# Kernel tuning notes

Measured on AMD Instinct MI355X. Metric: run time of the kernel, lower is better.

## Reference

```python
import jax, jax.numpy as jnp
import numpy as np

# ---- fixed architecture hyperparameters (match init_kwargs) ----
B, S = 4, 1024
L, H, DM, DF = 4, 8, 512, 2048
DH = DM // H          # 64 head dim (= 2*R after gated SPE filter)
NS = 5                # num_sines
R = 32                # num_realizations
M = 2 * DH            # favor_feature_dims = 128 (split as +/- of 64 projections)
LN_EPS = 1e-5
ATT_EPS = 1e-6


def layernorm(x, g, b):
    mu = x.mean(-1, keepdims=True)
    var = ((x - mu) ** 2).mean(-1, keepdims=True)
    return (x - mu) * jax.lax.rsqrt(var + LN_EPS) * g + b


def sine_spe(freqs, offsets, gains, noise, seq_len):
    """SineSPE positional code. freqs/offsets/gains: (H,DH,NS); noise: (H,DH,2NS,R).
    Returns qbar, kbar of shape (S,H,DH,R)."""
    pos = jnp.arange(seq_len, dtype=freqs.dtype)
    f = jax.nn.sigmoid(freqs)[:, :, None, :] / 2.0                       # (H,DH,1,NS)
    ph_q = 2.0 * jnp.pi * f * pos[None, None, :, None] + offsets[:, :, None, :]
    ph_k = 2.0 * jnp.pi * f * pos[None, None, :, None]
    om_q = jnp.stack([jnp.cos(ph_q), jnp.sin(ph_q)], -1).reshape(H, DH, seq_len, 2 * NS)
    om_k = jnp.stack([jnp.cos(ph_k), jnp.sin(ph_k)], -1).reshape(H, DH, seq_len, 2 * NS)
    g = jax.nn.softplus(gains)
    g = jnp.stack([g, g], -1).reshape(H, DH, 2 * NS)                      # upsample gains
    z = noise * g[..., None] / jnp.sqrt(jnp.asarray(2.0 * NS, freqs.dtype))
    qbar = jnp.einsum('hdsk,hdkr->shdr', om_q, z)
    kbar = jnp.einsum('hdsk,hdkr->shdr', om_k, z)
    scale = (R * DH) ** 0.25
    return qbar / scale, kbar / scale


def spe_filter(q, k, qbar, kbar, gate, gnoise):
    """Gated SPE filter. q,k: (B,S,H,DH); qbar/kbar: (S,H,DH,R); gate: (H,DH); gnoise: (H,DH,R).
    Returns qhat, khat of shape (B,S,H,2R)."""
    g = jax.nn.sigmoid(gate)[..., None]                                   # (H,DH,1)
    gn = gnoise / (DH * R) ** 0.25
    seq_len = qbar.shape[0]
    bias = jnp.broadcast_to(jnp.sqrt(g) * gn, (seq_len, H, DH, R))
    qb = jnp.concatenate([jnp.sqrt(1.0 - g) * qbar, bias], -1)            # (S,H,DH,2R)
    kb = jnp.concatenate([jnp.sqrt(1.0 - g) * kbar, bias], -1)
    qhat = jnp.einsum('bshd,shdr->bshr', q, qb)
    khat = jnp.einsum('bshd,shdr->bshr', k, kb)
    return qhat, khat


def favor(x, omega):
    """FAVOR+ softmax feature map. x: (B,S,H,DH); omega: (DH, M//2) -> (B,S,H,M)."""
    x = x * (DH ** -0.25)                                                 # sqrt(softmax_temp), temp=1/sqrt(DH)
    half_norm = 0.5 * jnp.sum(x * x, -1, keepdims=True)
    u = jnp.einsum('bshe,em->bshm', x, omega)
    phi = jnp.concatenate([jnp.exp(u - half_norm), jnp.exp(-u - half_norm)], -1)
    return phi / jnp.sqrt(jnp.asarray(M, x.dtype))


def causal_linear_attention(Q, K, V):
    """Causal linear (kernelized) attention via lax.scan. Q,K: (B,S,H,M); V: (B,S,H,DH)."""
    Bv = Q.shape[0]

    def step(carry, qkv):
        Skv, sk = carry
        q, k, v = qkv                                                     # (B,H,M),(B,H,M),(B,H,DH)
        Skv = Skv + jnp.einsum('bhm,bhd->bhmd', k, v)
        sk = sk + k
        num = jnp.einsum('bhm,bhmd->bhd', q, Skv)
        den = jnp.einsum('bhm,bhm->bh', q, sk) + ATT_EPS
        return (Skv, sk), num / den[..., None]

    init = (jnp.zeros((Bv, H, M, DH), Q.dtype), jnp.zeros((Bv, H, M), Q.dtype))
    xs = tuple(jnp.moveaxis(t, 1, 0) for t in (Q, K, V))
    _, out = jax.lax.scan(step, init, xs)
    return jnp.moveaxis(out, 0, 1)                                        # (B,S,H,DH)


def setup_inputs() -> dict:
    key = jax.random.key(0)
    ks = jax.random.split(key, 14)

    def rn(k, shape, scale=1.0):
        return jax.random.normal(k, shape, dtype=jnp.float32) * scale

    return {
        'x': rn(ks[0], (B, S, DM)),
        'Wq': rn(ks[1], (L, DM, DM), 0.02), 'bq': jnp.zeros((L, DM), jnp.float32),
        'Wk': rn(ks[2], (L, DM, DM), 0.02), 'bk': jnp.zeros((L, DM), jnp.float32),
        'Wv': rn(ks[3], (L, DM, DM), 0.02), 'bv': jnp.zeros((L, DM), jnp.float32),
        'Wo': rn(ks[4], (L, DM, DM), 0.02), 'bo': jnp.zeros((L, DM), jnp.float32),
        'W1': rn(ks[5], (L, DM, DF), 0.02), 'b1': jnp.zeros((L, DF), jnp.float32),
        'W2': rn(ks[6], (L, DF, DM), 0.02), 'b2': jnp.zeros((L, DM), jnp.float32),
        'ln1_g': jnp.ones((L, DM), jnp.float32), 'ln1_b': jnp.zeros((L, DM), jnp.float32),
        'ln2_g': jnp.ones((L, DM), jnp.float32), 'ln2_b': jnp.zeros((L, DM), jnp.float32),
        'spe_freqs': rn(ks[7], (L, H, DH, NS)),
        'spe_offsets': rn(ks[8], (L, H, DH, NS)),
        'spe_gains': rn(ks[9], (L, H, DH, NS)),
        'spe_noise': rn(ks[10], (L, H, DH, 2 * NS, R)),
        'gate': rn(ks[11], (L, H, DH)),
        'gate_noise': rn(ks[12], (L, H, DH, R)),
        'favor_omega': rn(ks[13], (L, DH, M // 2)),
    }


def reference(x, Wq, bq, Wk, bk, Wv, bv, Wo, bo, W1, b1, W2, b2,
              ln1_g, ln1_b, ln2_g, ln2_b,
              spe_freqs, spe_offsets, spe_gains, spe_noise, gate, gate_noise, favor_omega):
    Bv, Sv, _ = x.shape
    out = x
    for l in range(L):
        qbar, kbar = sine_spe(spe_freqs[l], spe_offsets[l], spe_gains[l], spe_noise[l], Sv)
        q = (out @ Wq[l] + bq[l]).reshape(Bv, Sv, H, DH)
        k = (out @ Wk[l] + bk[l]).reshape(Bv, Sv, H, DH)
        v = (out @ Wv[l] + bv[l]).reshape(Bv, Sv, H, DH)
        qh, kh = spe_filter(q, k, qbar, kbar, gate[l], gate_noise[l])
        Qf = favor(qh, favor_omega[l])
        Kf = favor(kh, favor_omega[l])
        att = causal_linear_attention(Qf, Kf, v).reshape(Bv, Sv, DM)
        att = att @ Wo[l] + bo[l]
        h = layernorm(out + att, ln1_g[l], ln1_b[l])
        y = jax.nn.relu(h @ W1[l] + b1[l]) @ W2[l] + b2[l]
        out = layernorm(h + y, ln2_g[l], ln2_b[l])
    return out
```

## Files before the change

### kernel.cpp

```cpp
#include <hip/hip_runtime.h>
#include <math.h>

#define BB 4
#define SS 1024
#define LL 4
#define HH 8
#define DM 512
#define DF 2048
#define DH 64
#define NS 5
#define RR 32
#define MM 128
#define NC 16
#define CHK 64
#define QKV_N 1536

#define INV_SQRT10   0.316227766016838f
#define INV_SCALE    0.148650889375340f
#define TEMP_SCALE   0.353553390593274f
#define INV_SQRT_M   0.088388347648318f
#define TWO_PI       6.283185307179586f

typedef __attribute__((ext_vector_type(8))) short bf16x8;
typedef __attribute__((ext_vector_type(4))) float f32x4;

__device__ __forceinline__ unsigned short f2bf(float f) {
  union { float f; unsigned int u; } v; v.f = f;
  unsigned int r = v.u + 0x7FFFu + ((v.u >> 16) & 1u);
  return (unsigned short)(r >> 16);
}

__device__ __forceinline__ float bf2f(unsigned short u) {
  union { unsigned int u; float f; } v; v.u = (unsigned int)u << 16;
  return v.f;
}

__device__ __forceinline__ void gld_lds16(const unsigned short* g, unsigned short* l) {
  __builtin_amdgcn_global_load_lds((const __attribute__((address_space(1))) void*)g,
                                   (__attribute__((address_space(3))) void*)l,
                                   16, 0, 0);
}

template<int RELU, int OUT_BF>
__global__ __launch_bounds__(256)
void gemm_mfma(const unsigned short* __restrict__ A, const unsigned short* __restrict__ Bt,
               const float* __restrict__ bias, float* __restrict__ Cf,
               unsigned short* __restrict__ Cbf, int M, int N, int K)
{
  __shared__ unsigned short As[128 * 32];
  __shared__ unsigned short Bs[128 * 32];
  const int tid  = threadIdx.x;
  const int w    = tid >> 6;
  const int lane = tid & 63;
  const int row0 = blockIdx.y * 128;
  const int col0 = blockIdx.x * 128;
  const int wr = (w >> 1) * 64;
  const int wc = (w & 1) * 64;
  const int c0 = w * 2, c1 = w * 2 + 1;
  const int m0 = c0 * 16 + (lane >> 2);
  const int m1 = c1 * 16 + (lane >> 2);
  const int kA = (lane & 3) * 8;

  f32x4 acc[4][4] = {};

  for (int k0 = 0; k0 < K; k0 += 32) {
    gld_lds16(&A [(size_t)(row0 + m0) * K + k0 + kA], &As[c0 * 512]);
    gld_lds16(&A [(size_t)(row0 + m1) * K + k0 + kA], &As[c1 * 512]);
    gld_lds16(&Bt[(size_t)(col0 + m0) * K + k0 + kA], &Bs[c0 * 512]);
    gld_lds16(&Bt[(size_t)(col0 + m1) * K + k0 + kA], &Bs[c1 * 512]);
    __syncthreads();
    const int rA = wr + (lane & 15);
    const int rB = wc + (lane & 15);
    const int kk = (lane >> 4) * 8;
    bf16x8 af[4], bfr[4];
#pragma unroll
    for (int i = 0; i < 4; ++i) {
      af[i]  = *reinterpret_cast<const bf16x8*>(&As[(rA + i * 16) * 32 + kk]);
      bfr[i] = *reinterpret_cast<const bf16x8*>(&Bs[(rB + i * 16) * 32 + kk]);
    }
#pragma unroll
    for (int mi = 0; mi < 4; ++mi)
#pragma unroll
      for (int ni = 0; ni < 4; ++ni)
        acc[mi][ni] = __builtin_amdgcn_mfma_f32_16x16x32_bf16(af[mi], bfr[ni], acc[mi][ni], 0, 0, 0);
    __syncthreads();
  }
  const int cr = (lane >> 4) * 4;
  const int cc = lane & 15;
#pragma unroll
  for (int mi = 0; mi < 4; ++mi) {
#pragma unroll
    for (int ni = 0; ni < 4; ++ni) {
      const int col = col0 + wc + ni * 16 + cc;
      const float bv = bias[col];
#pragma unroll
      for (int r = 0; r < 4; ++r) {
        const int row = row0 + wr + mi * 16 + cr + r;
        float v = acc[mi][ni][r] + bv;
        if (RELU) v = fmaxf(v, 0.f);
        if (OUT_BF) Cbf[(size_t)row * N + col] = f2bf(v);
        else        Cf [(size_t)row * N + col] = v;
      }
    }
  }
}

template<int RELU, int OUT_BF>
__global__ __launch_bounds__(256)
void gemm_mfma_n64(const unsigned short* __restrict__ A, const unsigned short* __restrict__ Bt,
                   const float* __restrict__ bias, float* __restrict__ Cf,
                   unsigned short* __restrict__ Cbf, int M, int N, int K)
{
  __shared__ unsigned short As[128 * 32];
  __shared__ unsigned short Bs[64 * 32];
  const int tid  = threadIdx.x;
  const int w    = tid >> 6;
  const int lane = tid & 63;
  const int row0 = blockIdx.y * 128;
  const int col0 = blockIdx.x * 64;
  const int wr = (w >> 1) * 64;
  const int wc = (w & 1) * 32;
  const int c0 = w * 2, c1 = w * 2 + 1;
  const int m0 = c0 * 16 + (lane >> 2);
  const int m1 = c1 * 16 + (lane >> 2);
  const int mb = w * 16 + (lane >> 2);
  const int kA = (lane & 3) * 8;

  f32x4 acc[4][2] = {};

  for (int k0 = 0; k0 < K; k0 += 32) {
    gld_lds16(&A [(size_t)(row0 + m0) * K + k0 + kA], &As[c0 * 512]);
    gld_lds16(&A [(size_t)(row0 + m1) * K + k0 + kA], &As[c1 * 512]);
    gld_lds16(&Bt[(size_t)(col0 + mb) * K + k0 + kA], &Bs[w * 512]);
    __syncthreads();
    const int rA = wr + (lane & 15);
    const int rB = wc + (lane & 15);
    const int kk = (lane >> 4) * 8;
    bf16x8 af[4], bfr[2];
#pragma unroll
    for (int i = 0; i < 4; ++i)
      af[i]  = *reinterpret_cast<const bf16x8*>(&As[(rA + i * 16) * 32 + kk]);
#pragma unroll
    for (int i = 0; i < 2; ++i)
      bfr[i] = *reinterpret_cast<const bf16x8*>(&Bs[(rB + i * 16) * 32 + kk]);
#pragma unroll
    for (int mi = 0; mi < 4; ++mi)
#pragma unroll
      for (int ni = 0; ni < 2; ++ni)
        acc[mi][ni] = __builtin_amdgcn_mfma_f32_16x16x32_bf16(af[mi], bfr[ni], acc[mi][ni], 0, 0, 0);
    __syncthreads();
  }
  const int cr = (lane >> 4) * 4;
  const int cc = lane & 15;
#pragma unroll
  for (int mi = 0; mi < 4; ++mi) {
#pragma unroll
    for (int ni = 0; ni < 2; ++ni) {
      const int col = col0 + wc + ni * 16 + cc;
      const float bv = bias[col];
#pragma unroll
      for (int r = 0; r < 4; ++r) {
        const int row = row0 + wr + mi * 16 + cr + r;
        float v = acc[mi][ni][r] + bv;
        if (RELU) v = fmaxf(v, 0.f);
        if (OUT_BF) Cbf[(size_t)row * N + col] = f2bf(v);
        else        Cf [(size_t)row * N + col] = v;
      }
    }
  }
}

__global__ __launch_bounds__(256)
void transpose_bf(const float* __restrict__ W, unsigned short* __restrict__ Wt, int K, int N,
                  size_t inStride, size_t outStride)
{
  const float* Wl = W + blockIdx.z * inStride;
  unsigned short* Wtl = Wt + blockIdx.z * outStride;
  __shared__ float tile[32][33];
  const int k0 = blockIdx.y * 32, n0 = blockIdx.x * 32;
  const int tx = threadIdx.x & 31, ty = threadIdx.x >> 5;
#pragma unroll
  for (int j = 0; j < 4; ++j)
    tile[ty + 8 * j][tx] = Wl[(size_t)(k0 + ty + 8 * j) * N + n0 + tx];
  __syncthreads();
#pragma unroll
  for (int j = 0; j < 4; ++j)
    Wtl[(size_t)(n0 + ty + 8 * j) * K + k0 + tx] = f2bf(tile[tx][ty + 8 * j]);
}

__global__ __launch_bounds__(256)
void pack_bias(const float* __restrict__ bq, const float* __restrict__ bk,
               const float* __restrict__ bv, float* __restrict__ out)
{
  const int l = blockIdx.y;
  const int i = blockIdx.x * 256 + threadIdx.x;
  if (i < QKV_N)
    out[l * QKV_N + i] = (i < 512) ? bq[l * DM + i] : (i < 1024) ? bk[l * DM + i - 512]
                                                                 : bv[l * DM + i - 1024];
}

__global__ __launch_bounds__(256)
void cvt_bf16(const float* __restrict__ in, unsigned short* __restrict__ out, int n4)
{
  const int i = blockIdx.x * 256 + threadIdx.x;
  if (i < n4) {
    const float4 v = reinterpret_cast<const float4*>(in)[i];
    ushort4 o;
    o.x = f2bf(v.x); o.y = f2bf(v.y); o.z = f2bf(v.z); o.w = f2bf(v.w);
    reinterpret_cast<ushort4*>(out)[i] = o;
  }
}

__global__ __launch_bounds__(256)
void spe_prep_all(const float* __restrict__ gains, const float* __restrict__ noise,
                  const float* __restrict__ gate, const float* __restrict__ gnoise,
                  const float* __restrict__ offsets,
                  float* __restrict__ zpf, unsigned short* __restrict__ wbb,
                  float2* __restrict__ offcs)
{
  const int i = blockIdx.x * 256 + threadIdx.x;
  const int NZ = LL * HH * RR * 10 * DH;
  const int NW = LL * HH * RR * DH;
  const int NO = LL * HH * DH * NS;
  if (i < NZ) {
    const int d = i & 63;
    int j = i >> 6;
    const int k = j % 10; j /= 10;
    const int r = j & 31; j >>= 5;
    const int h = j & 7;  const int l = j >> 3;
    const int lhd = (l * HH + h) * DH + d;
    const float ga = gains[lhd * NS + (k >> 1)];
    const float sp = (ga > 20.f) ? ga : log1pf(__expf(ga));
    const float gg = 1.f / (1.f + __expf(-gate[lhd]));
    const float c1 = sqrtf(fmaxf(1.f - gg, 0.f));
    const float nz = noise[((size_t)lhd * 10 + k) * 32 + r];
    zpf[i] = nz * sp * c1 * (INV_SQRT10 * INV_SCALE * TEMP_SCALE);
  } else if (i < NZ + NW) {
    int j = i - NZ;
    const int d = j & 63; j >>= 6;
    const int r = j & 31; j >>= 5;
    const int h = j & 7;  const int l = j >> 3;
    const int lhd = (l * HH + h) * DH + d;
    const float gg = 1.f / (1.f + __expf(-gate[lhd]));
    wbb[i - NZ] = f2bf(sqrtf(gg) * gnoise[(size_t)lhd * 32 + r] * (INV_SCALE * TEMP_SCALE));
  } else if (i < NZ + NW + NO) {
    const int j = i - NZ - NW;
    float sn, cn;
    __sincosf(offsets[j], &sn, &cn);
    offcs[j] = make_float2(cn, sn);
  }
}

__global__ __launch_bounds__(256)
void spe_xhat(const float* __restrict__ freqs, const float2* __restrict__ offcs,
              const float* __restrict__ zpf, const unsigned short* __restrict__ wbb,
              const unsigned short* __restrict__ qkvb,
              unsigned short* __restrict__ xhat, float* __restrict__ hn)
{
  const int s = blockIdx.x;
  const int h = blockIdx.y;
  const int t = threadIdx.x;
  const int w = t >> 6;
  const int lane = t & 63;
  __shared__ float omqT[10][64];
  __shared__ float omkT[10][64];
  __shared__ unsigned short qbT[64 * 64];
  __shared__ unsigned short kbT[64 * 64];
  __shared__ unsigned short rQ[16 * 64];
  __shared__ unsigned short rK[16 * 64];
  __shared__ float hqp[4][8];

  for (int e = t; e < DH * NS; e += 256) {
    const int d = e / NS, ns = e - d * NS;
    const float fr = 0.5f / (1.f + __expf(-freqs[(h * DH + d) * NS + ns]));
    float sn, cn;
    __sincosf(TWO_PI * fr * (float)s, &sn, &cn);
    const float2 oc = offcs[(h * DH + d) * NS + ns];
    omkT[2 * ns][d]     = cn;
    omkT[2 * ns + 1][d] = sn;
    omqT[2 * ns][d]     = cn * oc.x - sn * oc.y;
    omqT[2 * ns + 1][d] = sn * oc.x + cn * oc.y;
  }
  if (t < 64) {
    const int isK = t >> 5;
    const int b = (t >> 3) & 3;
    const int j = t & 7;
    const unsigned short* src = qkvb + ((size_t)b * SS + s) * QKV_N + isK * 512 + h * DH + j * 8;
    unsigned short* dst = (isK ? rK : rQ) + b * 64 + ((j ^ b) << 3);
    *reinterpret_cast<bf16x8*>(dst) = *reinterpret_cast<const bf16x8*>(src);
  } else if (t < 256) {
    const int i = t - 64;
    bf16x8 z = {};
    if (i < 96) *reinterpret_cast<bf16x8*>(&rQ[256 + i * 8]) = z;
    else        *reinterpret_cast<bf16x8*>(&rK[256 + (i - 96) * 8]) = z;
  }
  __syncthreads();
  {
    const int r = t >> 3, d0 = (t & 7) * 8;
    float accq[8] = {}, acck[8] = {};
    const float* zr = zpf + (size_t)(h * RR + r) * 640 + d0;
#pragma unroll
    for (int k = 0; k < 10; ++k) {
      const float4 z0 = *reinterpret_cast<const float4*>(zr + k * 64);
      const float4 z1 = *reinterpret_cast<const float4*>(zr + k * 64 + 4);
      const float4 oq0 = *reinterpret_cast<const float4*>(&omqT[k][d0]);
      const float4 oq1 = *reinterpret_cast<const float4*>(&omqT[k][d0 + 4]);
      const float4 ok0 = *reinterpret_cast<const float4*>(&omkT[k][d0]);
      const float4 ok1 = *reinterpret_cast<const float4*>(&omkT[k][d0 + 4]);
      accq[0] += z0.x * oq0.x; accq[1] += z0.y * oq0.y;
      accq[2] += z0.z * oq0.z; accq[3] += z0.w * oq0.w;
      accq[4] += z1.x * oq1.x; accq[5] += z1.y * oq1.y;
      accq[6] += z1.z * oq1.z; accq[7] += z1.w * oq1.w;
      acck[0] += z0.x * ok0.x; acck[1] += z0.y * ok0.y;
      acck[2] += z0.z * ok0.z; acck[3] += z0.w * ok0.w;
      acck[4] += z1.x * ok1.x; acck[5] += z1.y * ok1.y;
      acck[6] += z1.z * ok1.z; acck[7] += z1.w * ok1.w;
    }
    bf16x8 qv, kv;
#pragma unroll
    for (int j = 0; j < 8; ++j) {
      qv[j] = (short)f2bf(accq[j]);
      kv[j] = (short)f2bf(acck[j]);
    }
    const int sd0 = d0 ^ ((r & 7) << 3);
    *reinterpret_cast<bf16x8*>(&qbT[r * 64 + sd0]) = qv;
    *reinterpret_cast<bf16x8*>(&kbT[r * 64 + sd0]) = kv;
    const bf16x8 wv = *reinterpret_cast<const bf16x8*>(&wbb[(size_t)(h * RR + r) * 64 + d0]);
    *reinterpret_cast<bf16x8*>(&qbT[(32 + r) * 64 + sd0]) = wv;
    *reinterpret_cast<bf16x8*>(&kbT[(32 + r) * 64 + sd0]) = wv;
  }
  __syncthreads();
  f32x4 aq = {0.f, 0.f, 0.f, 0.f}, ak = {0.f, 0.f, 0.f, 0.f};
  const int arow = lane & 15;
  const int colr = w * 16 + (lane & 15);
#pragma unroll
  for (int kt = 0; kt < 2; ++kt) {
    const int g = kt * 4 + (lane >> 4);
    const bf16x8 fAq = *reinterpret_cast<const bf16x8*>(&rQ[arow * 64 + ((g ^ (arow & 7)) << 3)]);
    const bf16x8 fAk = *reinterpret_cast<const bf16x8*>(&rK[arow * 64 + ((g ^ (arow & 7)) << 3)]);
    const bf16x8 fBq = *reinterpret_cast<const bf16x8*>(&qbT[colr * 64 + ((g ^ (colr & 7)) << 3)]);
    const bf16x8 fBk = *reinterpret_cast<const bf16x8*>(&kbT[colr * 64 + ((g ^ (colr & 7)) << 3)]);
    aq = __builtin_amdgcn_mfma_f32_16x16x32_bf16(fAq, fBq, aq, 0, 0, 0);
    ak = __builtin_amdgcn_mfma_f32_16x16x32_bf16(fAk, fBk, ak, 0, 0, 0);
  }
  float rq[4], rk2[4];
#pragma unroll
  for (int r = 0; r < 4; ++r) { rq[r] = aq[r] * aq[r]; rk2[r] = ak[r] * ak[r]; }
#pragma unroll
  for (int off = 1; off < 16; off <<= 1) {
#pragma unroll
    for (int r = 0; r < 4; ++r) {
      rq[r]  += __shfl_xor(rq[r],  off, 64);
      rk2[r] += __shfl_xor(rk2[r], off, 64);
    }
  }
  if (lane == 0) {
#pragma unroll
    for (int r = 0; r < 4; ++r) { hqp[w][r] = rq[r]; hqp[w][4 + r] = rk2[r]; }
  }
  if (lane < 16) {
#pragma unroll
    for (int r = 0; r < 4; ++r) {
      const size_t rowq = ((size_t)r * SS + s) * HH + h;
      xhat[rowq * 64 + w * 16 + lane] = f2bf(aq[r]);
      xhat[(rowq + (size_t)BB * SS * HH) * 64 + w * 16 + lane] = f2bf(ak[r]);
    }
  }
  __syncthreads();
  if (t < 8) {
    const int b = t & 3;
    const int ko = (t >> 2) * 4;
    const float v = 0.5f * (hqp[0][ko + b] + hqp[1][ko + b] + hqp[2][ko + b] + hqp[3][ko + b]);
    const size_t row = ((size_t)b * SS + s) * HH + h + (size_t)(t >> 2) * BB * SS * HH;
    hn[row] = v;
  }
}

__global__ __launch_bounds__(256)
void favor_gemm(const unsigned short* __restrict__ xhat, const unsigned short* __restrict__ omgT,
                const float* __restrict__ hn, unsigned short* __restrict__ QfKfB)
{
  __shared__ unsigned short As[128 * 32];
  __shared__ unsigned short Bs[64 * 32];
  const int tid  = threadIdx.x;
  const int w    = tid >> 6;
  const int lane = tid & 63;
  const int row0 = blockIdx.x * 128;
  const int c0 = w * 2, c1 = w * 2 + 1;
  const int m0 = c0 * 16 + (lane >> 2);
  const int m1 = c1 * 16 + (lane >> 2);
  const int mb = w * 16 + (lane >> 2);
  const int kA = (lane & 3) * 8;

  f32x4 acc[2][4] = {};

  for (int k0 = 0; k0 < 64; k0 += 32) {
    gld_lds16(&xhat[(size_t)(row0 + m0) * 64 + k0 + kA], &As[c0 * 512]);
    gld_lds16(&xhat[(size_t)(row0 + m1) * 64 + k0 + kA], &As[c1 * 512]);
    gld_lds16(&omgT[(size_t)mb * 64 + k0 + kA], &Bs[w * 512]);
    __syncthreads();
    const int rA = w * 32 + (lane & 15);
    const int kk = (lane >> 4) * 8;
    bf16x8 af[2], bfr[4];
#pragma unroll
    for (int i = 0; i < 2; ++i)
      af[i]  = *reinterpret_cast<const bf16x8*>(&As[(rA + i * 16) * 32 + kk]);
#pragma unroll
    for (int i = 0; i < 4; ++i)
      bfr[i] = *reinterpret_cast<const bf16x8*>(&Bs[(i * 16 + (lane & 15)) * 32 + kk]);
#pragma unroll
    for (int mi = 0; mi < 2; ++mi)
#pragma unroll
      for (int ni = 0; ni < 4; ++ni)
        acc[mi][ni] = __builtin_amdgcn_mfma_f32_16x16x32_bf16(af[mi], bfr[ni], acc[mi][ni], 0, 0, 0);
    __syncthreads();
  }
  const int cr = (lane >> 4) * 4;
  const int cc = lane & 15;
#pragma unroll
  for (int mi = 0; mi < 2; ++mi) {
#pragma unroll
    for (int r = 0; r < 4; ++r) {
      const size_t row = row0 + w * 32 + mi * 16 + cr + r;
      const float hnv = hn[row];
#pragma unroll
      for (int ni = 0; ni < 4; ++ni) {
        const int m = ni * 16 + cc;
        const float u = acc[mi][ni][r];
        QfKfB[row * MM + m]      = f2bf(__expf( u - hnv) * INV_SQRT_M);
        QfKfB[row * MM + m + 64] = f2bf(__expf(-u - hnv) * INV_SQRT_M);
      }
    }
  }
}

__global__ __launch_bounds__(256)
void attn_chunk_sums(const unsigned short* __restrict__ KfB, const unsigned short* __restrict__ qkvb,
                     float* __restrict__ Sch, float* __restrict__ kch)
{
  const int c = blockIdx.x, h = blockIdx.y, b = blockIdx.z;
  const int tid = threadIdx.x;
  const int w = tid >> 6, lane = tid & 63;
  __shared__ unsigned short KcT[128 * 64];
  __shared__ unsigned short VT[64 * 64];
  const size_t srow0 = (size_t)b * SS + c * CHK;

  for (int i = tid; i < 1024; i += 256) {
    const int m = i & 127, oct = i >> 7;
    const unsigned short* src = KfB + ((srow0 + oct * 8) * HH + h) * MM + m;
    bf16x8 v;
#pragma unroll
    for (int j = 0; j < 8; ++j) v[j] = (short)src[(size_t)j * (HH * MM)];
    *reinterpret_cast<bf16x8*>(&KcT[m * 64 + ((oct << 3) ^ ((m & 7) << 3))]) = v;
  }
  for (int i = tid; i < 512; i += 256) {
    const int d = i & 63, oct = i >> 6;
    const unsigned short* src = qkvb + (srow0 + oct * 8) * QKV_N + 1024 + h * DH + d;
    bf16x8 v;
#pragma unroll
    for (int j = 0; j < 8; ++j) v[j] = (short)src[(size_t)j * QKV_N];
    *reinterpret_cast<bf16x8*>(&VT[d * 64 + ((oct << 3) ^ ((d & 7) << 3))]) = v;
  }
  __syncthreads();

  const int kk = (lane >> 4) * 8;
  f32x4 acc[4][2] = {};
#pragma unroll
  for (int kc = 0; kc < 2; ++kc) {
    const int k = kc * 32 + kk;
#pragma unroll
    for (int di = 0; di < 4; ++di) {
      const int dA = di * 16 + (lane & 15);
      const bf16x8 a = *reinterpret_cast<const bf16x8*>(&VT[dA * 64 + (k ^ ((dA & 7) << 3))]);
#pragma unroll
      for (int mi = 0; mi < 2; ++mi) {
        const int mB = w * 32 + mi * 16 + (lane & 15);
        const bf16x8 bb = *reinterpret_cast<const bf16x8*>(&KcT[mB * 64 + (k ^ ((mB & 7) << 3))]);
        acc[di][mi] = __builtin_amdgcn_mfma_f32_16x16x32_bf16(a, bb, acc[di][mi], 0, 0, 0);
      }
    }
  }
  const size_t base = (((size_t)b * HH + h) * NC + c);
  float* So = Sch + base * (MM * DH);
  const int cr = (lane >> 4) * 4, cc = lane & 15;
#pragma unroll
  for (int di = 0; di < 4; ++di)
#pragma unroll
    for (int mi = 0; mi < 2; ++mi)
#pragma unroll
      for (int r = 0; r < 4; ++r)
        So[(size_t)(di * 16 + cr + r) * MM + (w * 32 + mi * 16 + cc)] = acc[di][mi][r];
  {
    const int m = tid >> 1, half = tid & 1;
    float ks = 0.f;
#pragma unroll
    for (int j = 0; j < 32; ++j) {
      const int t2 = half * 32 + j;
      ks += bf2f(KcT[m * 64 + (t2 ^ ((m & 7) << 3))]);
    }
    ks += __shfl_xor(ks, 1, 64);
    if (half == 0) kch[base * MM + m] = ks;
  }
}

__global__ __launch_bounds__(256)
void attn_scan(float* __restrict__ Sch, float* __restrict__ kch)
{
  const int bh = blockIdx.x, part = blockIdx.y;
  const int t = threadIdx.x;
  float* base = Sch + (size_t)bh * NC * (MM * DH);
  for (int e = part * 1024 + t; e < (part + 1) * 1024; e += 256) {
    float run = 0.f;
#pragma unroll
    for (int c = 0; c < NC; ++c) {
      const float v = base[(size_t)c * (MM * DH) + e];
      base[(size_t)c * (MM * DH) + e] = run;
      run += v;
    }
  }
  if (part == 0 && t < MM) {
    float* kb2 = kch + (size_t)bh * NC * MM;
    float run = 0.f;
#pragma unroll
    for (int c = 0; c < NC; ++c) {
      const float v = kb2[c * MM + t];
      kb2[c * MM + t] = run;
      run += v;
    }
  }
}

__global__ __launch_bounds__(256)
void attn_out(const unsigned short* __restrict__ QfKfB, const unsigned short* __restrict__ qkvb,
              const float* __restrict__ Sch, const float* __restrict__ kch,
              unsigned short* __restrict__ att)
{
  const int c = blockIdx.x, h = blockIdx.y, b = blockIdx.z;
  const int tid = threadIdx.x;
  const int w = tid >> 6;
  const int lane = tid & 63;
  __shared__ unsigned short Qc[64 * 128];
  __shared__ unsigned short Sb[64 * 64];
  __shared__ unsigned short KVU[12288];
  __shared__ float skp[MM];
  __shared__ float denl[64];

  unsigned short* Kc   = KVU;
  unsigned short* SpxT = KVU;
  unsigned short* VT   = KVU + 8192;

  const size_t srow0 = (size_t)b * SS + c * CHK;
  const unsigned short* Qg = QfKfB + (srow0 * HH + h) * MM;
  const unsigned short* Kg = Qg + (size_t)BB * SS * HH * MM;

  if (tid < MM) skp[tid] = kch[(((size_t)b * HH + h) * NC + c) * MM + tid];

  for (int i = tid; i < 1024; i += 256) {
    const int s2 = i >> 4, m8 = (i & 15) * 8;
    const int sw = m8 ^ ((s2 & 15) << 3);
    *reinterpret_cast<bf16x8*>(&Qc[s2 * 128 + sw]) =
        *reinterpret_cast<const bf16x8*>(&Qg[(size_t)s2 * (HH * MM) + m8]);
    *reinterpret_cast<bf16x8*>(&Kc[s2 * 128 + sw]) =
        *reinterpret_cast<const bf16x8*>(&Kg[(size_t)s2 * (HH * MM) + m8]);
  }
  for (int i = tid; i < 512; i += 256) {
    const int d = i & 63, oct = i >> 6;
    const unsigned short* src = qkvb + (srow0 + oct * 8) * QKV_N + 1024 + h * DH + d;
    bf16x8 v;
#pragma unroll
    for (int j = 0; j < 8; ++j) v[j] = (short)src[(size_t)j * QKV_N];
    *reinterpret_cast<bf16x8*>(&VT[d * 64 + ((oct << 3) ^ ((d & 7) << 3))]) = v;
  }
  __syncthreads();

  const int sA = w * 16 + (lane & 15);
  const int kk = (lane >> 4) * 8;
  f32x4 acc_s[4] = {};
#pragma unroll
  for (int kc = 0; kc < 4; ++kc) {
    const int k = kc * 32 + kk;
    const bf16x8 aq = *reinterpret_cast<const bf16x8*>(&Qc[sA * 128 + (k ^ ((sA & 15) << 3))]);
#pragma unroll
    for (int n = 0; n < 4; ++n) {
      const int tB = n * 16 + (lane & 15);
      const bf16x8 bq = *reinterpret_cast<const bf16x8*>(&Kc[tB * 128 + (k ^ ((tB & 15) << 3))]);
      acc_s[n] = __builtin_amdgcn_mfma_f32_16x16x32_bf16(aq, bq, acc_s[n], 0, 0, 0);
    }
  }
  __syncthreads();

  {
    const int g = lane >> 4;
    const int tcol = lane & 15;
    float dintra[4] = {0.f, 0.f, 0.f, 0.f};
#pragma unroll
    for (int r = 0; r < 4; ++r) {
      const int s = w * 16 + g * 4 + r;
#pragma unroll
      for (int n = 0; n < 4; ++n) {
        const int t2 = n * 16 + tcol;
        const float v = (t2 <= s) ? acc_s[n][r] : 0.f;
        dintra[r] += v;
        Sb[s * 64 + (t2 ^ ((s & 7) << 3))] = f2bf(v);
      }
    }
#pragma unroll
    for (int off = 1; off < 16; off <<= 1)
#pragma unroll
      for (int r = 0; r < 4; ++r) dintra[r] += __shfl_xor(dintra[r], off, 64);
    if (tcol == 0) {
#pragma unroll
      for (int r = 0; r < 4; ++r) denl[w * 16 + g * 4 + r] = dintra[r];
    }
  }
  {
    const float* Sp = Sch + (((size_t)b * HH + h) * NC + c) * (MM * DH);
    for (int i = tid; i < 1024; i += 256) {
      const int d = i >> 4, mo = (i & 15) * 8;
      const float4 a0 = *reinterpret_cast<const float4*>(Sp + (size_t)d * MM + mo);
      const float4 a1 = *reinterpret_cast<const float4*>(Sp + (size_t)d * MM + mo + 4);
      bf16x8 v;
      v[0] = (short)f2bf(a0.x); v[1] = (short)f2bf(a0.y);
      v[2] = (short)f2bf(a0.z); v[3] = (short)f2bf(a0.w);
      v[4] = (short)f2bf(a1.x); v[5] = (short)f2bf(a1.y);
      v[6] = (short)f2bf(a1.z); v[7] = (short)f2bf(a1.w);
      *reinterpret_cast<bf16x8*>(&SpxT[d * 128 + (mo ^ ((d & 15) << 3))]) = v;
    }
  }
  __syncthreads();

  f32x4 acc_o[4] = {};
#pragma unroll
  for (int kc = 0; kc < 2; ++kc) {
    const int k = kc * 32 + kk;
    const bf16x8 as = *reinterpret_cast<const bf16x8*>(&Sb[sA * 64 + (k ^ ((sA & 7) << 3))]);
#pragma unroll
    for (int n = 0; n < 4; ++n) {
      const int dB = n * 16 + (lane & 15);
      const bf16x8 bv = *reinterpret_cast<const bf16x8*>(&VT[dB * 64 + (k ^ ((dB & 7) << 3))]);
      acc_o[n] = __builtin_amdgcn_mfma_f32_16x16x32_bf16(as, bv, acc_o[n], 0, 0, 0);
    }
  }
#pragma unroll
  for (int kc = 0; kc < 4; ++kc) {
    const int k = kc * 32 + kk;
    const bf16x8 aq = *reinterpret_cast<const bf16x8*>(&Qc[sA * 128 + (k ^ ((sA & 15) << 3))]);
#pragma unroll
    for (int n = 0; n < 4; ++n) {
      const int dB = n * 16 + (lane & 15);
      const bf16x8 bs = *reinterpret_cast<const bf16x8*>(&SpxT[dB * 128 + (k ^ ((dB & 15) << 3))]);
      acc_o[n] = __builtin_amdgcn_mfma_f32_16x16x32_bf16(aq, bs, acc_o[n], 0, 0, 0);
    }
  }
  {
    const int s2 = tid >> 2, part = tid & 3;
    float p = 0.f;
#pragma unroll
    for (int j = 0; j < 32; ++j) {
      const int m = part * 32 + j;
      p += bf2f(Qc[s2 * 128 + (m ^ ((s2 & 15) << 3))]) * skp[m];
    }
    p += __shfl_xor(p, 1, 64);
    p += __shfl_xor(p, 2, 64);
    if (part == 0) denl[s2] += p + 1e-6f;
  }
  __syncthreads();

  {
    const int g = lane >> 4;
    const int dcol = lane & 15;
#pragma unroll
    for (int r = 0; r < 4; ++r) {
      const int s = w * 16 + g * 4 + r;
      const float dinv = 1.f / denl[s];
#pragma unroll
      for (int n = 0; n < 4; ++n)
        att[(srow0 + s) * DM + h * DH + n * 16 + dcol] = f2bf(acc_o[n][r] * dinv);
    }
  }
}

template<int WBF>
__global__ __launch_bounds__(256)
void add_ln(const float* __restrict__ a, const float* __restrict__ bres,
            const float* __restrict__ g, const float* __restrict__ be,
            float* __restrict__ out, unsigned short* __restrict__ outbf)
{
  const int row = blockIdx.x;
  const int t = threadIdx.x;
  const size_t base = (size_t)row * DM;
  const float x0 = a[base + t] + bres[base + t];
  const float x1 = a[base + t + 256] + bres[base + t + 256];
  __shared__ float red[8];
  float ssum = x0 + x1;
#pragma unroll
  for (int off = 32; off > 0; off >>= 1) ssum += __shfl_xor(ssum, off, 64);
  const int wid = t >> 6, lid = t & 63;
  if (lid == 0) red[wid] = ssum;
  __syncthreads();
  const float mu = (red[0] + red[1] + red[2] + red[3]) * (1.f / DM);
  const float d0 = x0 - mu, d1 = x1 - mu;
  float sv = d0 * d0 + d1 * d1;
#pragma unroll
  for (int off = 32; off > 0; off >>= 1) sv += __shfl_xor(sv, off, 64);
  if (lid == 0) red[4 + wid] = sv;
  __syncthreads();
  const float var = (red[4] + red[5] + red[6] + red[7]) * (1.f / DM);
  const float rs = rsqrtf(var + 1e-5f);
  const float o0 = d0 * rs * g[t]       + be[t];
  const float o1 = d1 * rs * g[t + 256] + be[t + 256];
  out[base + t]       = o0;
  out[base + t + 256] = o1;
  if (WBF) {
    outbf[base + t]       = f2bf(o0);
    outbf[base + t + 256] = f2bf(o1);
  }
}

extern "C" void kernel_launch(void* const* d_in, const int* in_sizes, int n_in,
                              void* d_out, int out_size, void* d_ws, size_t ws_size,
                              hipStream_t stream)
{
  const float* x      = (const float*)d_in[0];
  const float* Wq     = (const float*)d_in[1];
  const float* bq     = (const float*)d_in[2];
  const float* Wk     = (const float*)d_in[3];
  const float* bk     = (const float*)d_in[4];
  const float* Wv     = (const float*)d_in[5];
  const float* bv     = (const float*)d_in[6];
  const float* Wo     = (const float*)d_in[7];
  const float* bo     = (const float*)d_in[8];
  const float* W1     = (const float*)d_in[9];
  const float* b1     = (const float*)d_in[10];
  const float* W2     = (const float*)d_in[11];
  const float* b2     = (const float*)d_in[12];
  const float* ln1g   = (const float*)d_in[13];
  const float* ln1b   = (const float*)d_in[14];
  const float* ln2g   = (const float*)d_in[15];
  const float* ln2b   = (const float*)d_in[16];
  const float* freqs  = (const float*)d_in[17];
  const float* offs   = (const float*)d_in[18];
  const float* gains  = (const float*)d_in[19];
  const float* noise  = (const float*)d_in[20];
  const float* gate   = (const float*)d_in[21];
  const float* gnoise = (const float*)d_in[22];
  const float* omega  = (const float*)d_in[23];

  float* ws = (float*)d_ws;
  size_t o = 0;
  float* curf = ws + o; o += (size_t)BB * SS * DM;
  unsigned short* qkvb = (unsigned short*)(ws + o); o += (size_t)BB * SS * QKV_N / 2;
  float* Sch  = ws + o; o += (size_t)BB * HH * NC * MM * DH;
  float* kch  = ws + o; o += (size_t)BB * HH * NC * MM;
  float* hn   = ws + o; o += (size_t)2 * BB * SS * HH;
  float* bqkv = ws + o; o += (size_t)LL * QKV_N;
  float2* offcs = (float2*)(ws + o); o += (size_t)LL * HH * DH * NS * 2;
  float* zpf  = ws + o; o += (size_t)LL * HH * RR * 10 * DH;
  unsigned short* QfKfB = (unsigned short*)(ws + o); o += (size_t)2 * BB * SS * HH * MM / 2;
  unsigned short* xhat  = (unsigned short*)(ws + o); o += (size_t)2 * BB * SS * HH * DH / 2;
  unsigned short* attb  = (unsigned short*)(ws + o); o += (size_t)BB * SS * DM / 2;
  unsigned short* h_bf  = (unsigned short*)(ws + o); o += (size_t)BB * SS * DM / 2;
  unsigned short* curbf = (unsigned short*)(ws + o); o += (size_t)BB * SS * DM / 2;
  unsigned short* Wqkvt = (unsigned short*)(ws + o); o += (size_t)LL * QKV_N * DM / 2;
  unsigned short* Wot   = (unsigned short*)(ws + o); o += (size_t)LL * DM * DM / 2;
  unsigned short* W1t   = (unsigned short*)(ws + o); o += (size_t)DF * DM / 2;
  unsigned short* W2t   = (unsigned short*)(ws + o); o += (size_t)DM * DF / 2;
  unsigned short* omgT  = (unsigned short*)(ws + o); o += (size_t)LL * 4096 / 2;
  unsigned short* wbb   = (unsigned short*)(ws + o); o += (size_t)LL * HH * RR * DH / 2;

  float* attp = (float*)qkvb;
  float* hbuf = Sch;
  float* ybuf = Sch + (size_t)2 * 1024 * 1024;
  unsigned short* midbf = QfKfB;
  unsigned short* KfB   = QfKfB + (size_t)BB * SS * HH * MM;

  const int MROWS = BB * SS;

  cvt_bf16<<<(BB * SS * DM / 4 + 255) / 256, 256, 0, stream>>>(x, curbf, BB * SS * DM / 4);
  spe_prep_all<<<2856, 256, 0, stream>>>(gains, noise, gate, gnoise, offs, zpf, wbb, offcs);
  transpose_bf<<<dim3(16, 16, 4), 256, 0, stream>>>(Wq, Wqkvt,                     DM, DM, (size_t)DM * DM, (size_t)QKV_N * DM);
  transpose_bf<<<dim3(16, 16, 4), 256, 0, stream>>>(Wk, Wqkvt + (size_t)512 * DM,  DM, DM, (size_t)DM * DM, (size_t)QKV_N * DM);
  transpose_bf<<<dim3(16, 16, 4), 256, 0, stream>>>(Wv, Wqkvt + (size_t)1024 * DM, DM, DM, (size_t)DM * DM, (size_t)QKV_N * DM);
  transpose_bf<<<dim3(16, 16, 4), 256, 0, stream>>>(Wo, Wot, DM, DM, (size_t)DM * DM, (size_t)DM * DM);
  transpose_bf<<<dim3(2, 2, 4),   256, 0, stream>>>(omega, omgT, DH, MM / 2, (size_t)DH * (MM / 2), 4096);
  pack_bias<<<dim3(6, 4), 256, 0, stream>>>(bq, bk, bv, bqkv);

  for (int l = 0; l < LL; ++l) {
    const float* in = (l == 0) ? x : curf;

    gemm_mfma_n64<0, 1><<<dim3(QKV_N / 64, MROWS / 128), 256, 0, stream>>>(
        curbf, Wqkvt + (size_t)l * QKV_N * DM, bqkv + (size_t)l * QKV_N,
        (float*)nullptr, qkvb, MROWS, QKV_N, DM);

    spe_xhat<<<dim3(SS, HH), 256, 0, stream>>>(
        freqs + (size_t)l * HH * DH * NS, offcs + (size_t)l * HH * DH * NS,
        zpf + (size_t)l * HH * RR * 10 * DH, wbb + (size_t)l * HH * RR * DH,
        qkvb, xhat, hn);
    favor_gemm<<<dim3(2 * BB * SS * HH / 128), 256, 0, stream>>>(
        xhat, omgT + (size_t)l * 4096, hn, QfKfB);

    attn_chunk_sums<<<dim3(NC, HH, BB), 256, 0, stream>>>(KfB, qkvb, Sch, kch);
    attn_scan<<<dim3(BB * HH, 8), 256, 0, stream>>>(Sch, kch);
    attn_out<<<dim3(NC, HH, BB), 256, 0, stream>>>(QfKfB, qkvb, Sch, kch, attb);

    gemm_mfma_n64<0, 0><<<dim3(DM / 64, MROWS / 128), 256, 0, stream>>>(
        attb, Wot + (size_t)l * DM * DM, bo + (size_t)l * DM,
        attp, (unsigned short*)nullptr, MROWS, DM, DM);

    add_ln<1><<<MROWS, 256, 0, stream>>>(in, attp, ln1g + (size_t)l * DM, ln1b + (size_t)l * DM, hbuf, h_bf);

    transpose_bf<<<dim3(64, 16, 1), 256, 0, stream>>>(W1 + (size_t)l * DM * DF, W1t, DM, DF, 0, 0);
    gemm_mfma<1, 1><<<dim3(DF / 128, MROWS / 128), 256, 0, stream>>>(
        h_bf, W1t, b1 + (size_t)l * DF, (float*)nullptr, midbf, MROWS, DF, DM);
    transpose_bf<<<dim3(16, 64, 1), 256, 0, stream>>>(W2 + (size_t)l * DF * DM, W2t, DF, DM, 0, 0);
    gemm_mfma_n64<0, 0><<<dim3(DM / 64, MROWS / 128), 256, 0, stream>>>(
        midbf, W2t, b2 + (size_t)l * DM, ybuf, (unsigned short*)nullptr, MROWS, DM, DF);

    if (l == LL - 1) {
      add_ln<0><<<MROWS, 256, 0, stream>>>(hbuf, ybuf, ln2g + (size_t)l * DM, ln2b + (size_t)l * DM,
                                           (float*)d_out, (unsigned short*)nullptr);
    } else {
      add_ln<1><<<MROWS, 256, 0, stream>>>(hbuf, ybuf, ln2g + (size_t)l * DM, ln2b + (size_t)l * DM,
                                           curf, curbf);
    }
  }
}
```

Before: 747.9 us.

## Process eight positions per spe_xhat block with LDS-staged bf16 SPE noise

Each spe_xhat block now handles SG=8 consecutive sequence positions instead of one. The per-head z-matrix is stored pre-swizzled in bf16 and loaded once into LDS via gld_lds16, then reused across the eight positions. The sine/cosine terms are advanced with an angle-addition recurrence instead of a fresh sincos per position. This cuts repeated global z loads, the fp32 z traffic and transcendental work, but leaves only 1024 blocks, adds about 40KB of LDS per block (lowering occupancy), serialises positions with barriers, and adds bf16 rounding to z plus recurrence drift.

```diff
diff --git a/kernel.cpp b/kernel.cpp
--- a/kernel.cpp
+++ b/kernel.cpp
@@ -14,6 +14,7 @@
 #define NC 16
 #define CHK 64
 #define QKV_N 1536
+#define SG 8
 
 #define INV_SQRT10   0.316227766016838f
 #define INV_SCALE    0.148650889375340f
@@ -215,7 +216,7 @@
 void spe_prep_all(const float* __restrict__ gains, const float* __restrict__ noise,
                   const float* __restrict__ gate, const float* __restrict__ gnoise,
                   const float* __restrict__ offsets,
-                  float* __restrict__ zpf, unsigned short* __restrict__ wbb,
+                  unsigned short* __restrict__ zpb, unsigned short* __restrict__ wbb,
                   float2* __restrict__ offcs)
 {
   const int i = blockIdx.x * 256 + threadIdx.x;
@@ -234,7 +235,8 @@
     const float gg = 1.f / (1.f + __expf(-gate[lhd]));
     const float c1 = sqrtf(fmaxf(1.f - gg, 0.f));
     const float nz = noise[((size_t)lhd * 10 + k) * 32 + r];
-    zpf[i] = nz * sp * c1 * (INV_SQRT10 * INV_SCALE * TEMP_SCALE);
+    const int dsw = d ^ ((r & 7) << 3);
+    zpb[(i & ~63) | dsw] = f2bf(nz * sp * c1 * (INV_SQRT10 * INV_SCALE * TEMP_SCALE));
   } else if (i < NZ + NW) {
     int j = i - NZ;
     const int d = j & 63; j >>= 6;
@@ -253,125 +255,162 @@
 
 __global__ __launch_bounds__(256)
 void spe_xhat(const float* __restrict__ freqs, const float2* __restrict__ offcs,
-              const float* __restrict__ zpf, const unsigned short* __restrict__ wbb,
+              const unsigned short* __restrict__ zpb, const unsigned short* __restrict__ wbb,
               const unsigned short* __restrict__ qkvb,
               unsigned short* __restrict__ xhat, float* __restrict__ hn)
 {
-  const int s = blockIdx.x;
-  const int h = blockIdx.y;
-  const int t = threadIdx.x;
-  const int w = t >> 6;
+  const int s0 = blockIdx.x * SG;
+  const int h  = blockIdx.y;
+  const int t  = threadIdx.x;
+  const int w  = t >> 6;
   const int lane = t & 63;
+
+  __shared__ unsigned short zbS[RR * 10 * DH];
   __shared__ float omqT[10][64];
   __shared__ float omkT[10][64];
   __shared__ unsigned short qbT[64 * 64];
   __shared__ unsigned short kbT[64 * 64];
-  __shared__ unsigned short rQ[16 * 64];
-  __shared__ unsigned short rK[16 * 64];
-  __shared__ float hqp[4][8];
-
-  for (int e = t; e < DH * NS; e += 256) {
-    const int d = e / NS, ns = e - d * NS;
-    const float fr = 0.5f / (1.f + __expf(-freqs[(h * DH + d) * NS + ns]));
-    float sn, cn;
-    __sincosf(TWO_PI * fr * (float)s, &sn, &cn);
-    const float2 oc = offcs[(h * DH + d) * NS + ns];
-    omkT[2 * ns][d]     = cn;
-    omkT[2 * ns + 1][d] = sn;
-    omqT[2 * ns][d]     = cn * oc.x - sn * oc.y;
-    omqT[2 * ns + 1][d] = sn * oc.x + cn * oc.y;
-  }
+  __shared__ unsigned short rQall[SG][4][64];
+  __shared__ unsigned short rKall[SG][4][64];
+  __shared__ float hqp[SG][4][8];
+
+  {
+    const unsigned short* zsrc = zpb + (size_t)h * (RR * 10 * DH);
+#pragma unroll
+    for (int i = 0; i < 10; ++i)
+      gld_lds16(&zsrc[(size_t)(i * 256 + t) * 8], &zbS[(i * 256 + w * 64) * 8]);
+  }
+  for (int i = t; i < SG * 4 * 2 * 8; i += 256) {
+    const int oct = i & 7, qk = (i >> 3) & 1, b = (i >> 4) & 3, s = i >> 6;
+    const unsigned short* src = qkvb + ((size_t)b * SS + s0 + s) * QKV_N + qk * 512 + h * DH + oct * 8;
+    unsigned short* dst = (qk ? &rKall[s][b][0] : &rQall[s][b][0]) + ((oct ^ b) << 3);
+    *reinterpret_cast<bf16x8*>(dst) = *reinterpret_cast<const bf16x8*>(src);
+  }
+  {
+    const int r = t >> 3, oct = t & 7;
+    const bf16x8 wv = *reinterpret_cast<const bf16x8*>(&wbb[((size_t)h * RR + r) * 64 + oct * 8]);
+    const int sd = (oct ^ (r & 7)) << 3;
+    *reinterpret_cast<bf16x8*>(&qbT[(32 + r) * 64 + sd]) = wv;
+    *reinterpret_cast<bf16x8*>(&kbT[(32 + r) * 64 + sd]) = wv;
+  }
+  float ck[NS], sk[NS], cw[NS], sw[NS], ocx[NS], ocy[NS];
   if (t < 64) {
-    const int isK = t >> 5;
-    const int b = (t >> 3) & 3;
-    const int j = t & 7;
-    const unsigned short* src = qkvb + ((size_t)b * SS + s) * QKV_N + isK * 512 + h * DH + j * 8;
-    unsigned short* dst = (isK ? rK : rQ) + b * 64 + ((j ^ b) << 3);
-    *reinterpret_cast<bf16x8*>(dst) = *reinterpret_cast<const bf16x8*>(src);
-  } else if (t < 256) {
-    const int i = t - 64;
-    bf16x8 z = {};
-    if (i < 96) *reinterpret_cast<bf16x8*>(&rQ[256 + i * 8]) = z;
-    else        *reinterpret_cast<bf16x8*>(&rK[256 + (i - 96) * 8]) = z;
+    const int d = t;
+#pragma unroll
+    for (int ns = 0; ns < NS; ++ns) {
+      const float fr = 0.5f / (1.f + __expf(-freqs[(h * DH + d) * NS + ns]));
+      const float om = TWO_PI * fr;
+      __sincosf(om * (float)s0, &sk[ns], &ck[ns]);
+      __sincosf(om, &sw[ns], &cw[ns]);
+      const float2 oc = offcs[(h * DH + d) * NS + ns];
+      ocx[ns] = oc.x; ocy[ns] = oc.y;
+      omkT[2 * ns][d]     = ck[ns];
+      omkT[2 * ns + 1][d] = sk[ns];
+      omqT[2 * ns][d]     = ck[ns] * oc.x - sk[ns] * oc.y;
+      omqT[2 * ns + 1][d] = sk[ns] * oc.x + ck[ns] * oc.y;
+    }
   }
   __syncthreads();
-  {
-    const int r = t >> 3, d0 = (t & 7) * 8;
-    float accq[8] = {}, acck[8] = {};
-    const float* zr = zpf + (size_t)(h * RR + r) * 640 + d0;
-#pragma unroll
-    for (int k = 0; k < 10; ++k) {
-      const float4 z0 = *reinterpret_cast<const float4*>(zr + k * 64);
-      const float4 z1 = *reinterpret_cast<const float4*>(zr + k * 64 + 4);
-      const float4 oq0 = *reinterpret_cast<const float4*>(&omqT[k][d0]);
-      const float4 oq1 = *reinterpret_cast<const float4*>(&omqT[k][d0 + 4]);
-      const float4 ok0 = *reinterpret_cast<const float4*>(&omkT[k][d0]);
-      const float4 ok1 = *reinterpret_cast<const float4*>(&omkT[k][d0 + 4]);
-      accq[0] += z0.x * oq0.x; accq[1] += z0.y * oq0.y;
-      accq[2] += z0.z * oq0.z; accq[3] += z0.w * oq0.w;
-      accq[4] += z1.x * oq1.x; accq[5] += z1.y * oq1.y;
-      accq[6] += z1.z * oq1.z; accq[7] += z1.w * oq1.w;
-      acck[0] += z0.x * ok0.x; acck[1] += z0.y * ok0.y;
-      acck[2] += z0.z * ok0.z; acck[3] += z0.w * ok0.w;
-      acck[4] += z1.x * ok1.x; acck[5] += z1.y * ok1.y;
-      acck[6] += z1.z * ok1.z; acck[7] += z1.w * ok1.w;
-    }
-    bf16x8 qv, kv;
-#pragma unroll
-    for (int j = 0; j < 8; ++j) {
-      qv[j] = (short)f2bf(accq[j]);
-      kv[j] = (short)f2bf(acck[j]);
-    }
-    const int sd0 = d0 ^ ((r & 7) << 3);
-    *reinterpret_cast<bf16x8*>(&qbT[r * 64 + sd0]) = qv;
-    *reinterpret_cast<bf16x8*>(&kbT[r * 64 + sd0]) = kv;
-    const bf16x8 wv = *reinterpret_cast<const bf16x8*>(&wbb[(size_t)(h * RR + r) * 64 + d0]);
-    *reinterpret_cast<bf16x8*>(&qbT[(32 + r) * 64 + sd0]) = wv;
-    *reinterpret_cast<bf16x8*>(&kbT[(32 + r) * 64 + sd0]) = wv;
-  }
-  __syncthreads();
-  f32x4 aq = {0.f, 0.f, 0.f, 0.f}, ak = {0.f, 0.f, 0.f, 0.f};
+
   const int arow = lane & 15;
+  const int brow = arow & 3;
   const int colr = w * 16 + (lane & 15);
-#pragma unroll
-  for (int kt = 0; kt < 2; ++kt) {
-    const int g = kt * 4 + (lane >> 4);
-    const bf16x8 fAq = *reinterpret_cast<const bf16x8*>(&rQ[arow * 64 + ((g ^ (arow & 7)) << 3)]);
-    const bf16x8 fAk = *reinterpret_cast<const bf16x8*>(&rK[arow * 64 + ((g ^ (arow & 7)) << 3)]);
-    const bf16x8 fBq = *reinterpret_cast<const bf16x8*>(&qbT[colr * 64 + ((g ^ (colr & 7)) << 3)]);
-    const bf16x8 fBk = *reinterpret_cast<const bf16x8*>(&kbT[colr * 64 + ((g ^ (colr & 7)) << 3)]);
-    aq = __builtin_amdgcn_mfma_f32_16x16x32_bf16(fAq, fBq, aq, 0, 0, 0);
-    ak = __builtin_amdgcn_mfma_f32_16x16x32_bf16(fAk, fBk, ak, 0, 0, 0);
-  }
-  float rq[4], rk2[4];
-#pragma unroll
-  for (int r = 0; r < 4; ++r) { rq[r] = aq[r] * aq[r]; rk2[r] = ak[r] * ak[r]; }
-#pragma unroll
-  for (int off = 1; off < 16; off <<= 1) {
-#pragma unroll
-    for (int r = 0; r < 4; ++r) {
-      rq[r]  += __shfl_xor(rq[r],  off, 64);
-      rk2[r] += __shfl_xor(rk2[r], off, 64);
-    }
-  }
-  if (lane == 0) {
-#pragma unroll
-    for (int r = 0; r < 4; ++r) { hqp[w][r] = rq[r]; hqp[w][4 + r] = rk2[r]; }
-  }
-  if (lane < 16) {
-#pragma unroll
-    for (int r = 0; r < 4; ++r) {
-      const size_t rowq = ((size_t)r * SS + s) * HH + h;
-      xhat[rowq * 64 + w * 16 + lane] = f2bf(aq[r]);
-      xhat[(rowq + (size_t)BB * SS * HH) * 64 + w * 16 + lane] = f2bf(ak[r]);
-    }
-  }
-  __syncthreads();
-  if (t < 8) {
-    const int b = t & 3;
-    const int ko = (t >> 2) * 4;
-    const float v = 0.5f * (hqp[0][ko + b] + hqp[1][ko + b] + hqp[2][ko + b] + hqp[3][ko + b]);
-    const size_t row = ((size_t)b * SS + s) * HH + h + (size_t)(t >> 2) * BB * SS * HH;
+
+  for (int si = 0; si < SG; ++si) {
+    {
+      const int r = t >> 3, oct = t & 7, d0 = oct * 8;
+      float accq[8] = {}, acck[8] = {};
+      const unsigned short* zr = &zbS[r * 640 + ((oct ^ (r & 7)) << 3)];
+#pragma unroll
+      for (int k = 0; k < 10; ++k) {
+        const bf16x8 zv = *reinterpret_cast<const bf16x8*>(&zr[k * 64]);
+        float zf[8];
+#pragma unroll
+        for (int j = 0; j < 8; ++j) zf[j] = bf2f((unsigned short)zv[j]);
+        const float4 oq0 = *reinterpret_cast<const float4*>(&omqT[k][d0]);
+        const float4 oq1 = *reinterpret_cast<const float4*>(&omqT[k][d0 + 4]);
+        const float4 ok0 = *reinterpret_cast<const float4*>(&omkT[k][d0]);
+        const float4 ok1 = *reinterpret_cast<const float4*>(&omkT[k][d0 + 4]);
+        accq[0] += zf[0] * oq0.x; accq[1] += zf[1] * oq0.y;
+        accq[2] += zf[2] * oq0.z; accq[3] += zf[3] * oq0.w;
+        accq[4] += zf[4] * oq1.x; accq[5] += zf[5] * oq1.y;
+        accq[6] += zf[6] * oq1.z; accq[7] += zf[7] * oq1.w;
+        acck[0] += zf[0] * ok0.x; acck[1] += zf[1] * ok0.y;
+        acck[2] += zf[2] * ok0.z; acck[3] += zf[3] * ok0.w;
+        acck[4] += zf[4] * ok1.x; acck[5] += zf[5] * ok1.y;
+        acck[6] += zf[6] * ok1.z; acck[7] += zf[7] * ok1.w;
+      }
+      bf16x8 qv, kv;
+#pragma unroll
+      for (int j = 0; j < 8; ++j) {
+        qv[j] = (short)f2bf(accq[j]);
+        kv[j] = (short)f2bf(acck[j]);
+      }
+      const int sd0 = d0 ^ ((r & 7) << 3);
+      *reinterpret_cast<bf16x8*>(&qbT[r * 64 + sd0]) = qv;
+      *reinterpret_cast<bf16x8*>(&kbT[r * 64 + sd0]) = kv;
+    }
+    __syncthreads();
+
+    f32x4 aq = {0.f, 0.f, 0.f, 0.f}, ak = {0.f, 0.f, 0.f, 0.f};
+    const bf16x8 zerov = {};
+#pragma unroll
+    for (int kt = 0; kt < 2; ++kt) {
+      const int g = kt * 4 + (lane >> 4);
+      const bf16x8 rq = *reinterpret_cast<const bf16x8*>(&rQall[si][brow][(g ^ brow) << 3]);
+      const bf16x8 rk = *reinterpret_cast<const bf16x8*>(&rKall[si][brow][(g ^ brow) << 3]);
+      const bf16x8 fAq = (arow < 4) ? rq : zerov;
+      const bf16x8 fAk = (arow < 4) ? rk : zerov;
+      const bf16x8 fBq = *reinterpret_cast<const bf16x8*>(&qbT[colr * 64 + ((g ^ (colr & 7)) << 3)]);
+      const bf16x8 fBk = *reinterpret_cast<const bf16x8*>(&kbT[colr * 64 + ((g ^ (colr & 7)) << 3)]);
+      aq = __builtin_amdgcn_mfma_f32_16x16x32_bf16(fAq, fBq, aq, 0, 0, 0);
+      ak = __builtin_amdgcn_mfma_f32_16x16x32_bf16(fAk, fBk, ak, 0, 0, 0);
+    }
+    {
+      float rq2[4], rk2[4];
+#pragma unroll
+      for (int r = 0; r < 4; ++r) { rq2[r] = aq[r] * aq[r]; rk2[r] = ak[r] * ak[r]; }
+#pragma unroll
+      for (int off = 1; off < 16; off <<= 1) {
+#pragma unroll
+        for (int r = 0; r < 4; ++r) {
+          rq2[r] += __shfl_xor(rq2[r], off, 64);
+          rk2[r] += __shfl_xor(rk2[r], off, 64);
+        }
+      }
+      if (lane == 0) {
+#pragma unroll
+        for (int r = 0; r < 4; ++r) { hqp[si][w][r] = rq2[r]; hqp[si][w][4 + r] = rk2[r]; }
+      }
+    }
+    if (lane < 16) {
+#pragma unroll
+      for (int r = 0; r < 4; ++r) {
+        const size_t rowq = ((size_t)r * SS + s0 + si) * HH + h;
+        xhat[rowq * 64 + w * 16 + lane] = f2bf(aq[r]);
+        xhat[(rowq + (size_t)BB * SS * HH) * 64 + w * 16 + lane] = f2bf(ak[r]);
+      }
+    }
+    if (si < SG - 1 && t < 64) {
+      const int d = t;
+#pragma unroll
+      for (int ns = 0; ns < NS; ++ns) {
+        const float c2 = ck[ns] * cw[ns] - sk[ns] * sw[ns];
+        const float s2 = sk[ns] * cw[ns] + ck[ns] * sw[ns];
+        ck[ns] = c2; sk[ns] = s2;
+        omkT[2 * ns][d]     = c2;
+        omkT[2 * ns + 1][d] = s2;
+        omqT[2 * ns][d]     = c2 * ocx[ns] - s2 * ocy[ns];
+        omqT[2 * ns + 1][d] = s2 * ocx[ns] + c2 * ocy[ns];
+      }
+    }
+    __syncthreads();
+  }
+
+  if (t < 64) {
+    const int si = t >> 3, j = t & 7, qk = j >> 2, b = j & 3;
+    const float v = 0.5f * (hqp[si][0][j] + hqp[si][1][j] + hqp[si][2][j] + hqp[si][3][j]);
+    const size_t row = ((size_t)b * SS + s0 + si) * HH + h + (size_t)qk * (BB * SS * HH);
     hn[row] = v;
   }
 }
@@ -755,7 +794,7 @@
   float* hn   = ws + o; o += (size_t)2 * BB * SS * HH;
   float* bqkv = ws + o; o += (size_t)LL * QKV_N;
   float2* offcs = (float2*)(ws + o); o += (size_t)LL * HH * DH * NS * 2;
-  float* zpf  = ws + o; o += (size_t)LL * HH * RR * 10 * DH;
+  unsigned short* zpb = (unsigned short*)(ws + o); o += (size_t)LL * HH * RR * 10 * DH / 2;
   unsigned short* QfKfB = (unsigned short*)(ws + o); o += (size_t)2 * BB * SS * HH * MM / 2;
   unsigned short* xhat  = (unsigned short*)(ws + o); o += (size_t)2 * BB * SS * HH * DH / 2;
   unsigned short* attb  = (unsigned short*)(ws + o); o += (size_t)BB * SS * DM / 2;
@@ -777,7 +816,7 @@
   const int MROWS = BB * SS;
 
   cvt_bf16<<<(BB * SS * DM / 4 + 255) / 256, 256, 0, stream>>>(x, curbf, BB * SS * DM / 4);
-  spe_prep_all<<<2856, 256, 0, stream>>>(gains, noise, gate, gnoise, offs, zpf, wbb, offcs);
+  spe_prep_all<<<2856, 256, 0, stream>>>(gains, noise, gate, gnoise, offs, zpb, wbb, offcs);
   transpose_bf<<<dim3(16, 16, 4), 256, 0, stream>>>(Wq, Wqkvt,                     DM, DM, (size_t)DM * DM, (size_t)QKV_N * DM);
   transpose_bf<<<dim3(16, 16, 4), 256, 0, stream>>>(Wk, Wqkvt + (size_t)512 * DM,  DM, DM, (size_t)DM * DM, (size_t)QKV_N * DM);
   transpose_bf<<<dim3(16, 16, 4), 256, 0, stream>>>(Wv, Wqkvt + (size_t)1024 * DM, DM, DM, (size_t)DM * DM, (size_t)QKV_N * DM);
@@ -792,9 +831,9 @@
         curbf, Wqkvt + (size_t)l * QKV_N * DM, bqkv + (size_t)l * QKV_N,
         (float*)nullptr, qkvb, MROWS, QKV_N, DM);
 
-    spe_xhat<<<dim3(SS, HH), 256, 0, stream>>>(
+    spe_xhat<<<dim3(SS / SG, HH), 256, 0, stream>>>(
         freqs + (size_t)l * HH * DH * NS, offcs + (size_t)l * HH * DH * NS,
-        zpf + (size_t)l * HH * RR * 10 * DH, wbb + (size_t)l * HH * RR * DH,
+        zpb + (size_t)l * HH * RR * 10 * DH, wbb + (size_t)l * HH * RR * DH,
         qkvb, xhat, hn);
     favor_gemm<<<dim3(2 * BB * SS * HH / 128), 256, 0, stream>>>(
         xhat, omgT + (size_t)l * 4096, hn, QfKfB);
```

After: 756.8 us. Within noise of the previous version (+1.2%).
